# Kernel optimization log

Measured on AMD Instinct MI355X. Metric: run time of the kernel, lower is better.

## Reference

```python
import jax, jax.numpy as jnp
import numpy as np

HID = 1024
HEADS = 16
DH = HID // HEADS
SCALE = DH ** -0.5
L, B = 2048, 2


def setup_inputs() -> dict:
    key = jax.random.key(0)
    ks = jax.random.split(key, 16)
    inp = {
        "query": jax.random.normal(ks[0], (L, B, HID), jnp.float32),
        "key": jax.random.normal(ks[1], (L, B, HID), jnp.float32),
        "value": jax.random.normal(ks[2], (L, B, HID), jnp.float32),
        "mask": jax.random.randint(ks[3], (B, L), 0, 2).astype(bool),
    }
    # xavier-uniform linear weights (torch Linear stores [out, in]; y = x @ W.T + b)
    lim = (6.0 / (HID + HID)) ** 0.5
    for i, name in enumerate(["wq", "wk", "wv", "wfc"]):
        inp[name] = jax.random.uniform(ks[4 + i], (HID, HID), jnp.float32, -lim, lim)
    inp["bq"] = jnp.zeros((HID,), jnp.float32)
    inp["bk"] = jnp.zeros((HID,), jnp.float32)
    inp["bv"] = jnp.zeros((HID,), jnp.float32)
    inp["bfc"] = jnp.zeros((HID,), jnp.float32)
    inp["tao"] = jnp.full((HEADS,), 10.0, jnp.float32)
    return inp


def reference(query, key, value, mask, wq, bq, wk, bk, wv, bv, wfc, bfc, tao):
    # inputs arrive [L, B, D]; module transposes to [B, L, D]
    q = jnp.swapaxes(query, 0, 1)
    k = jnp.swapaxes(key, 0, 1)
    v = jnp.swapaxes(value, 0, 1)
    bsz, length, _ = q.shape

    def heads(x, w, b):
        y = x @ w.T + b                      # [B, L, D]
        return y.reshape(bsz, length, HEADS, DH).transpose(0, 2, 1, 3)  # [B, H, L, d]

    Q = heads(q, wq, bq)
    K = heads(k, wk, bk)
    V = heads(v, wv, bv)

    qk = jnp.einsum("bhqd,bhkd->bhqk", Q, K) * SCALE  # [B, H, L, L]

    # gaussian positional bias: -|i-j|^2/2 * tao_h^-4
    idx = jnp.arange(length, dtype=jnp.float32)
    dist = -0.5 * (idx[:, None] - idx[None, :]) ** 2          # [L, L]
    qk = qk + dist[None, None, :, :] * (tao ** -4)[None, :, None, None]

    qk = jnp.where(mask[:, None, None, :], -jnp.inf, qk)
    attn = jax.nn.softmax(qk, axis=-1)  # dropout is identity in eval mode

    x = jnp.einsum("bhqk,bhkd->bhqd", attn, V)            # [B, H, L, d]
    x = x.transpose(0, 2, 1, 3).reshape(bsz, length, HID)  # [B, L, D]
    x = x @ wfc.T + bfc
    return jnp.swapaxes(x, 0, 1)  # [L, B, D]
```

## Files before the change

### kernel.cpp

```cpp
#include <hip/hip_runtime.h>

#define LQ   2048
#define BQ   2
#define HID  1024
#define NH   16
#define DH   64
#define SCALE 0.125f
#define L2E  1.44269504088896f
#define C1   0.18033688011f
#define EXPOFF 23.0831206542f

using short8  = __attribute__((ext_vector_type(8))) short;
using ushort8 = __attribute__((ext_vector_type(8))) unsigned short;
using f32x4   = __attribute__((ext_vector_type(4))) float;
typedef unsigned short u16;
typedef __attribute__((ext_vector_type(2))) __bf16 bf16x2;

__device__ inline u16 f2bf(float x) {
    unsigned int u = __float_as_uint(x);
    u = (u + 0x7fffu + ((u >> 16) & 1u)) >> 16;
    return (u16)u;
}

#if defined(__has_builtin)
#if __has_builtin(__builtin_amdgcn_cvt_pk_bf16_f32)
#define HAVE_PKBF 1
#endif
#if __has_builtin(__builtin_amdgcn_exp2f)
#define HAVE_EXP2 1
#endif
#endif

__device__ inline unsigned int pkbf(float a, float b) {
#ifdef HAVE_PKBF
    bf16x2 r = __builtin_amdgcn_cvt_pk_bf16_f32(a, b);
    return __builtin_bit_cast(unsigned int, r);
#else
    return (unsigned int)f2bf(a) | ((unsigned int)f2bf(b) << 16);
#endif
}

__device__ inline float fexp2(float x) {
#ifdef HAVE_EXP2
    return __builtin_amdgcn_exp2f(x);
#else
    return exp2f(x);
#endif
}

__device__ inline void gl_lds16(const void* g, void* l) {
    __builtin_amdgcn_global_load_lds(
        (const __attribute__((address_space(1))) void*)g,
        (__attribute__((address_space(3))) void*)l, 16, 0, 0);
}

struct CastArgs {
    const float* s[4];
    u16* d[4];
    int n;
    const unsigned char* mraw;
    int* mout;
    int mn;
};

__global__ __launch_bounds__(256) void castw(CastArgs a) {
    const int y = blockIdx.y;
    const int t = threadIdx.x;
    if (y == 4) {
        if (blockIdx.x != 0) return;
        __shared__ int cnt;
        if (t == 0) cnt = 0;
        __syncthreads();
        int local = 0;
        for (int i = t; i < a.mn; i += 256)
            if ((i & 3) && a.mraw[i]) local++;
        atomicAdd(&cnt, local);
        __syncthreads();
        bool isInt32 = (cnt == 0);
        const int* mi = (const int*)a.mraw;
        for (int i = t; i < a.mn; i += 256)
            a.mout[i] = isInt32 ? mi[i] : (int)a.mraw[i];
        return;
    }
    const float* s = a.s[y];
    u16* d = a.d[y];
    const int n4 = a.n >> 2;
    for (int i = blockIdx.x * 256 + t; i < n4; i += gridDim.x * 256) {
        float4 v = *(const float4*)(s + (size_t)i * 4);
        uint2 p;
        p.x = pkbf(v.x, v.y);
        p.y = pkbf(v.z, v.w);
        *(uint2*)(d + (size_t)i * 4) = p;
    }
}

struct QkvArgs {
    const float* A[3];
    const u16* W[3];
    const float* bias[3];
    u16* out[3];
};

__global__ __launch_bounds__(256) void gemm_qkv(QkvArgs ga) {
    __shared__ float Asf[128][32];
    __shared__ u16 Bs[128][32];

    const int z = blockIdx.z;
    const float* A = ga.A[z];
    const u16* W = ga.W[z];
    const float* bias = ga.bias[z];
    u16* outp = ga.out[z];

    const int t = threadIdx.x;
    const int m0 = blockIdx.x * 128;
    const int n0 = blockIdx.y * 128;
    const int lane = t & 63;
    const int lane15 = lane & 15;
    const int quad = lane >> 4;
    const int w = t >> 6;
    const int wm = (w >> 1) * 64;
    const int wn = (w & 1) * 64;

    const int arow = 8 * w + (lane >> 3);
    const int ach = (lane & 7) ^ ((lane >> 3) & 7);
    const float* aS = A + (size_t)(m0 + arow) * HID + 4 * ach;
    const int brow = 32 * w + (lane >> 2);
    const int bch = (lane & 3) ^ ((lane >> 3) & 3);
    const u16* bS0 = W + (size_t)(n0 + brow) * HID + 8 * bch;
    const u16* bS1 = bS0 + (size_t)16 * HID;
    u16* bD0 = &Bs[32 * w][0];
    u16* bD1 = &Bs[32 * w + 16][0];

    const int sa = lane15 & 7;
    const int qp = quad ^ ((lane15 >> 1) & 3);

    f32x4 acc[4][4];
#pragma unroll
    for (int i = 0; i < 4; i++)
#pragma unroll
        for (int j = 0; j < 4; j++) acc[i][j] = (f32x4){0,0,0,0};

    for (int k0 = 0; k0 < HID; k0 += 32) {
        __syncthreads();
#pragma unroll
        for (int i = 0; i < 4; i++)
            gl_lds16(aS + (size_t)(32 * i) * HID + k0, &Asf[32 * i + (8 * w)][0]);
        gl_lds16(bS0 + k0, bD0);
        gl_lds16(bS1 + k0, bD1);
        __syncthreads();

        short8 af[4], bf[4];
#pragma unroll
        for (int i = 0; i < 4; i++) {
            const float* ap = &Asf[wm + i * 16 + lane15][0];
            const float4 fa = *(const float4*)(ap + 4 * ((2 * quad) ^ sa));
            const float4 fb = *(const float4*)(ap + 4 * ((2 * quad + 1) ^ sa));
            uint4 ui;
            ui.x = pkbf(fa.x, fa.y); ui.y = pkbf(fa.z, fa.w);
            ui.z = pkbf(fb.x, fb.y); ui.w = pkbf(fb.z, fb.w);
            af[i] = __builtin_bit_cast(short8, ui);
            bf[i] = *(const short8*)&Bs[wn + i * 16 + lane15][qp * 8];
        }
#pragma unroll
        for (int mi = 0; mi < 4; mi++)
#pragma unroll
            for (int ni = 0; ni < 4; ni++)
                acc[mi][ni] = __builtin_amdgcn_mfma_f32_16x16x32_bf16(af[mi], bf[ni], acc[mi][ni], 0, 0, 0);
    }

#pragma unroll
    for (int mi = 0; mi < 4; mi++) {
#pragma unroll
        for (int ni = 0; ni < 4; ni++) {
            const int n = n0 + wn + ni * 16 + lane15;
            const float bv = bias[n];
            const int h = n >> 6, d = n & 63;
#pragma unroll
            for (int r = 0; r < 4; r++) {
                const int m = m0 + wm + mi * 16 + quad * 4 + r;
                const float c = acc[mi][ni][r] + bv;
                const int b = m & 1, l = m >> 1;
                if (z < 2) {
                    outp[(((size_t)(b * NH + h)) * LQ + l) * DH + d] = f2bf(c);
                } else {
                    outp[(((size_t)(b * NH + h)) * DH + d) * LQ + l] = f2bf(c);
                }
            }
        }
    }
}

__global__ __launch_bounds__(256) void gemm_fc(const u16* __restrict__ A,
                                               const u16* __restrict__ W,
                                               const float* __restrict__ bias,
                                               float* __restrict__ outp) {
    __shared__ u16 As[128][32];
    __shared__ u16 Bs[64][32];

    const int t = threadIdx.x;
    const int m0 = blockIdx.x * 128;
    const int n0 = blockIdx.y * 64;
    const int lane = t & 63;
    const int lane15 = lane & 15;
    const int quad = lane >> 4;
    const int w = t >> 6;
    const int wm = (w >> 1) * 64;
    const int wn = (w & 1) * 32;

    const int l4 = lane >> 2;
    const int ch = (lane & 3) ^ ((lane >> 3) & 3);
    const u16* aSrc0 = A + (size_t)(m0 + 32 * w + l4) * HID + 8 * ch;
    const u16* aSrc1 = aSrc0 + (size_t)16 * HID;
    const u16* bSrc0 = W + (size_t)(n0 + 16 * w + l4) * HID + 8 * ch;
    u16* aDst0 = &As[32 * w][0];
    u16* aDst1 = &As[32 * w + 16][0];
    u16* bDst0 = &Bs[16 * w][0];

    const int qp = quad ^ ((lane15 >> 1) & 3);

    f32x4 acc[4][2];
#pragma unroll
    for (int i = 0; i < 4; i++)
#pragma unroll
        for (int j = 0; j < 2; j++) acc[i][j] = (f32x4){0,0,0,0};

    for (int k0 = 0; k0 < HID; k0 += 32) {
        __syncthreads();
        gl_lds16(aSrc0 + k0, aDst0);
        gl_lds16(aSrc1 + k0, aDst1);
        gl_lds16(bSrc0 + k0, bDst0);
        __syncthreads();

        short8 af[4], bf[2];
#pragma unroll
        for (int i = 0; i < 4; i++)
            af[i] = *(const short8*)&As[wm + i * 16 + lane15][qp * 8];
#pragma unroll
        for (int j = 0; j < 2; j++)
            bf[j] = *(const short8*)&Bs[wn + j * 16 + lane15][qp * 8];
#pragma unroll
        for (int mi = 0; mi < 4; mi++)
#pragma unroll
            for (int ni = 0; ni < 2; ni++)
                acc[mi][ni] = __builtin_amdgcn_mfma_f32_16x16x32_bf16(af[mi], bf[ni], acc[mi][ni], 0, 0, 0);
    }

#pragma unroll
    for (int mi = 0; mi < 4; mi++) {
#pragma unroll
        for (int ni = 0; ni < 2; ni++) {
            const int n = n0 + wn + ni * 16 + lane15;
            const float bv = bias[n];
#pragma unroll
            for (int r = 0; r < 4; r++) {
                const int m = m0 + wm + mi * 16 + quad * 4 + r;
                outp[(size_t)m * HID + n] = acc[mi][ni][r] + bv;
            }
        }
    }
}

#define PSTR 72

__global__ __launch_bounds__(512) void attn_kernel(const u16* __restrict__ Qg,
                                                   const u16* __restrict__ Kg,
                                                   const u16* __restrict__ Vtg,
                                                   const int* __restrict__ maskI,
                                                   const float* __restrict__ tao,
                                                   u16* __restrict__ Xa) {
    __shared__ u16 Ks[128][64];
    __shared__ u16 Vt[64][128];
    __shared__ u16 PT[128][PSTR];
    __shared__ float smask[128];

    const int bh = blockIdx.x;
    const int q0 = blockIdx.y * 128;
    const int b = bh >> 4;
    const int h = bh & 15;
    const int t = threadIdx.x;
    const int w = t >> 6;
    const int lane = t & 63;
    const int lane15 = lane & 15;
    const int quad = lane >> 4;

    const u16* Kbase = Kg + (size_t)bh * LQ * DH;
    const u16* Vtbase = Vtg + (size_t)bh * DH * LQ;
    const int* mrow = maskI + b * LQ;

    const float tv = tao[h];
    const float t2 = tv * tv;
    const float nb = -0.5f / (t2 * t2);
    const float nb2 = nb * L2E;
    const float skipd2 = -40.0f / nb2;

    const int qrow = q0 + w * 16 + lane15;
    short8 qB0, qB1;
    {
        const u16* qp_ = Qg + ((size_t)bh * LQ + qrow) * DH + quad * 8;
        qB0 = *(const short8*)(qp_);
        qB1 = *(const short8*)(qp_ + 32);
    }

    const int krow = 8 * w + (lane >> 3);
    const int kch = (lane & 7) ^ ((lane >> 3) & 7);
    const u16* kS = Kbase + (size_t)krow * DH + 8 * kch;
    const int vrow = 4 * w + (lane >> 4);
    const int vch = (lane & 8) | ((lane & 7) ^ (vrow & 7));
    const u16* vS = Vtbase + (size_t)vrow * LQ + 8 * vch;
    u16* kD0 = &Ks[8 * w][0];
    u16* kD1 = &Ks[64 + 8 * w][0];
    u16* vD0 = &Vt[4 * w][0];
    u16* vD1 = &Vt[32 + 4 * w][0];

    const int s0 = (quad ^ (lane15 & 7)) * 8;
    const int s1 = ((4 + quad) ^ (lane15 & 7)) * 8;

    f32x4 O[4];
#pragma unroll
    for (int mt = 0; mt < 4; mt++) O[mt] = (f32x4){0,0,0,0};
    float l_ = 0.0f;

    const float ebase0 = (float)(qrow - quad * 4);
    const int prow = w * 16 + lane15;

    for (int k0 = 0; k0 < LQ; k0 += 128) {
        {
            int dmin = 0;
            if (k0 > q0 + 127) dmin = k0 - (q0 + 127);
            else if (k0 + 127 < q0) dmin = q0 - (k0 + 127);
            const float df = (float)dmin;
            if (df * df > skipd2) continue;
        }
        __syncthreads();
        gl_lds16(kS + (size_t)k0 * DH, kD0);
        gl_lds16(kS + (size_t)(k0 + 64) * DH, kD1);
        gl_lds16(vS + k0, vD0);
        gl_lds16(vS + (size_t)32 * LQ + k0, vD1);
        if (t < 128) smask[t] = mrow[k0 + t] ? -3.0e38f : -EXPOFF;
        __syncthreads();

#pragma unroll
        for (int hh = 0; hh < 2; hh++) {
            const int kbase = 64 * hh;
            f32x4 S[4];
#pragma unroll
            for (int kt = 0; kt < 4; kt++) {
                const u16* kr = &Ks[kbase + kt * 16 + lane15][0];
                const short8 ka = *(const short8*)(kr + s0);
                const short8 kb = *(const short8*)(kr + s1);
                S[kt] = __builtin_amdgcn_mfma_f32_16x16x32_bf16(ka, qB0, (f32x4){0,0,0,0}, 0, 0, 0);
                S[kt] = __builtin_amdgcn_mfma_f32_16x16x32_bf16(kb, qB1, S[kt], 0, 0, 0);
            }

            const float ebase = ebase0 - (float)(k0 + kbase);
            float lacc = 0.0f;
#pragma unroll
            for (int kt = 0; kt < 4; kt++) {
                const float4 sm4 = *(const float4*)&smask[kbase + kt * 16 + quad * 4];
                float p[4];
#pragma unroll
                for (int r = 0; r < 4; r++) {
                    const float d = ebase - (float)(kt * 16 + r);
                    const float tb = fmaf(nb2 * d, d, ((const float*)&sm4)[r]);
                    p[r] = fexp2(fmaf(S[kt][r], C1, tb));
                    lacc += p[r];
                }
                uint2 pk2;
                pk2.x = pkbf(p[0], p[1]);
                pk2.y = pkbf(p[2], p[3]);
                *(uint2*)&PT[prow][kt * 16 + quad * 4] = pk2;
            }
            l_ += lacc;

            const short8 pB0 = *(const short8*)&PT[prow][quad * 8];
            const short8 pB1 = *(const short8*)&PT[prow][32 + quad * 8];
#pragma unroll
            for (int mt = 0; mt < 4; mt++) {
                const u16* vr = &Vt[mt * 16 + lane15][kbase];
                const short8 va = *(const short8*)(vr + s0);
                const short8 vb = *(const short8*)(vr + s1);
                O[mt] = __builtin_amdgcn_mfma_f32_16x16x32_bf16(va, pB0, O[mt], 0, 0, 0);
                O[mt] = __builtin_amdgcn_mfma_f32_16x16x32_bf16(vb, pB1, O[mt], 0, 0, 0);
            }
        }
    }

    l_ += __shfl_xor(l_, 16, 64);
    l_ += __shfl_xor(l_, 32, 64);

    {
        const float inv = 1.0f / l_;
        u16* dst = Xa + ((size_t)qrow * BQ + b) * HID + h * DH;
#pragma unroll
        for (int mt = 0; mt < 4; mt++) {
            uint2 pk2;
            pk2.x = pkbf(O[mt][0] * inv, O[mt][1] * inv);
            pk2.y = pkbf(O[mt][2] * inv, O[mt][3] * inv);
            *(uint2*)(dst + mt * 16 + quad * 4) = pk2;
        }
    }
}

extern "C" void kernel_launch(void* const* d_in, const int* in_sizes, int n_in,
                              void* d_out, int out_size, void* d_ws, size_t ws_size,
                              hipStream_t stream) {
    const float* q    = (const float*)d_in[0];
    const float* k    = (const float*)d_in[1];
    const float* v    = (const float*)d_in[2];
    const void*  mask = d_in[3];
    const float* wq   = (const float*)d_in[4];
    const float* wk   = (const float*)d_in[5];
    const float* wv   = (const float*)d_in[6];
    const float* wfc  = (const float*)d_in[7];
    const float* bq   = (const float*)d_in[8];
    const float* bk   = (const float*)d_in[9];
    const float* bv   = (const float*)d_in[10];
    const float* bfc  = (const float*)d_in[11];
    const float* tao  = (const float*)d_in[12];

    const size_t NE = (size_t)LQ * BQ * HID;
    const size_t NW = (size_t)HID * HID;
    u16* base = (u16*)d_ws;
    u16* Qp    = base;
    u16* Kp    = base + NE;
    u16* Vtp   = base + 2 * NE;
    u16* Xa    = base + 3 * NE;
    u16* wqbf  = base + 4 * NE;
    u16* wkbf  = wqbf + NW;
    u16* wvbf  = wkbf + NW;
    u16* wfcbf = wvbf + NW;
    int* maskI = (int*)(wfcbf + NW);

    CastArgs ca;
    ca.s[0] = wq;  ca.d[0] = wqbf;
    ca.s[1] = wk;  ca.d[1] = wkbf;
    ca.s[2] = wv;  ca.d[2] = wvbf;
    ca.s[3] = wfc; ca.d[3] = wfcbf;
    ca.n = (int)NW;
    ca.mraw = (const unsigned char*)mask;
    ca.mout = maskI;
    ca.mn = BQ * LQ;
    castw<<<dim3(256, 5), 256, 0, stream>>>(ca);

    QkvArgs ga;
    ga.A[0] = q;  ga.W[0] = wqbf;  ga.bias[0] = bq;  ga.out[0] = Qp;
    ga.A[1] = k;  ga.W[1] = wkbf;  ga.bias[1] = bk;  ga.out[1] = Kp;
    ga.A[2] = v;  ga.W[2] = wvbf;  ga.bias[2] = bv;  ga.out[2] = Vtp;
    gemm_qkv<<<dim3(32, 8, 3), 256, 0, stream>>>(ga);

    attn_kernel<<<dim3(32, 16), 512, 0, stream>>>(Qp, Kp, Vtp, maskI, tao, Xa);

    gemm_fc<<<dim3(32, 16), 256, 0, stream>>>(Xa, wfcbf, bfc, (float*)d_out);
}
```

Baseline: 245.7 us.

## Pre-cast QKV activations to bf16 and deepen GEMM K-tiles to 64

The q/k/v activations are now converted to bf16 in the existing cast kernel, so the QKV GEMM loads bf16 instead of fp32 and no longer packs to bf16 inside its inner loop. Both the QKV and FC GEMMs move from a K-step of 32 to 64 with a new XOR swizzle, which halves the barrier count and issues two MFMAs per fragment pair. The trade-off is an extra full read and write pass over the activations in the cast kernel, plus more LDS per block.

```diff
diff --git a/kernel.cpp b/kernel.cpp
--- a/kernel.cpp
+++ b/kernel.cpp
@@ -55,9 +55,9 @@
 }
 
 struct CastArgs {
-    const float* s[4];
-    u16* d[4];
-    int n;
+    const float* s[7];
+    u16* d[7];
+    int n[7];
     const unsigned char* mraw;
     int* mout;
     int mn;
@@ -66,7 +66,7 @@
 __global__ __launch_bounds__(256) void castw(CastArgs a) {
     const int y = blockIdx.y;
     const int t = threadIdx.x;
-    if (y == 4) {
+    if (y == 7) {
         if (blockIdx.x != 0) return;
         __shared__ int cnt;
         if (t == 0) cnt = 0;
@@ -84,7 +84,7 @@
     }
     const float* s = a.s[y];
     u16* d = a.d[y];
-    const int n4 = a.n >> 2;
+    const int n4 = a.n[y] >> 2;
     for (int i = blockIdx.x * 256 + t; i < n4; i += gridDim.x * 256) {
         float4 v = *(const float4*)(s + (size_t)i * 4);
         uint2 p;
@@ -95,18 +95,18 @@
 }
 
 struct QkvArgs {
-    const float* A[3];
+    const u16* A[3];
     const u16* W[3];
     const float* bias[3];
     u16* out[3];
 };
 
 __global__ __launch_bounds__(256) void gemm_qkv(QkvArgs ga) {
-    __shared__ float Asf[128][32];
-    __shared__ u16 Bs[128][32];
+    __shared__ u16 As[128][64];
+    __shared__ u16 Bs[128][64];
 
     const int z = blockIdx.z;
-    const float* A = ga.A[z];
+    const u16* A = ga.A[z];
     const u16* W = ga.W[z];
     const float* bias = ga.bias[z];
     u16* outp = ga.out[z];
@@ -121,18 +121,13 @@
     const int wm = (w >> 1) * 64;
     const int wn = (w & 1) * 64;
 
-    const int arow = 8 * w + (lane >> 3);
-    const int ach = (lane & 7) ^ ((lane >> 3) & 7);
-    const float* aS = A + (size_t)(m0 + arow) * HID + 4 * ach;
-    const int brow = 32 * w + (lane >> 2);
-    const int bch = (lane & 3) ^ ((lane >> 3) & 3);
-    const u16* bS0 = W + (size_t)(n0 + brow) * HID + 8 * bch;
-    const u16* bS1 = bS0 + (size_t)16 * HID;
-    u16* bD0 = &Bs[32 * w][0];
-    u16* bD1 = &Bs[32 * w + 16][0];
-
-    const int sa = lane15 & 7;
-    const int qp = quad ^ ((lane15 >> 1) & 3);
+    const int lrow = lane >> 3;
+    const int ch = (lane & 7) ^ ((lane >> 3) & 7);
+    const u16* aS = A + (size_t)(m0 + 32 * w + lrow) * HID + 8 * ch;
+    const u16* bS = W + (size_t)(n0 + 32 * w + lrow) * HID + 8 * ch;
+
+    const int s0 = (quad ^ (lane15 & 7)) * 8;
+    const int s1 = ((4 + quad) ^ (lane15 & 7)) * 8;
 
     f32x4 acc[4][4];
 #pragma unroll
@@ -140,32 +135,32 @@
 #pragma unroll
         for (int j = 0; j < 4; j++) acc[i][j] = (f32x4){0,0,0,0};
 
-    for (int k0 = 0; k0 < HID; k0 += 32) {
-        __syncthreads();
-#pragma unroll
-        for (int i = 0; i < 4; i++)
-            gl_lds16(aS + (size_t)(32 * i) * HID + k0, &Asf[32 * i + (8 * w)][0]);
-        gl_lds16(bS0 + k0, bD0);
-        gl_lds16(bS1 + k0, bD1);
-        __syncthreads();
-
-        short8 af[4], bf[4];
+    for (int k0 = 0; k0 < HID; k0 += 64) {
+        __syncthreads();
 #pragma unroll
         for (int i = 0; i < 4; i++) {
-            const float* ap = &Asf[wm + i * 16 + lane15][0];
-            const float4 fa = *(const float4*)(ap + 4 * ((2 * quad) ^ sa));
-            const float4 fb = *(const float4*)(ap + 4 * ((2 * quad + 1) ^ sa));
-            uint4 ui;
-            ui.x = pkbf(fa.x, fa.y); ui.y = pkbf(fa.z, fa.w);
-            ui.z = pkbf(fb.x, fb.y); ui.w = pkbf(fb.z, fb.w);
-            af[i] = __builtin_bit_cast(short8, ui);
-            bf[i] = *(const short8*)&Bs[wn + i * 16 + lane15][qp * 8];
+            gl_lds16(aS + (size_t)(8 * i) * HID + k0, &As[32 * w + 8 * i][0]);
+            gl_lds16(bS + (size_t)(8 * i) * HID + k0, &Bs[32 * w + 8 * i][0]);
+        }
+        __syncthreads();
+
+        short8 af0[4], af1[4], bf0[4], bf1[4];
+#pragma unroll
+        for (int i = 0; i < 4; i++) {
+            const u16* ar = &As[wm + i * 16 + lane15][0];
+            const u16* br = &Bs[wn + i * 16 + lane15][0];
+            af0[i] = *(const short8*)(ar + s0);
+            af1[i] = *(const short8*)(ar + s1);
+            bf0[i] = *(const short8*)(br + s0);
+            bf1[i] = *(const short8*)(br + s1);
         }
 #pragma unroll
         for (int mi = 0; mi < 4; mi++)
 #pragma unroll
-            for (int ni = 0; ni < 4; ni++)
-                acc[mi][ni] = __builtin_amdgcn_mfma_f32_16x16x32_bf16(af[mi], bf[ni], acc[mi][ni], 0, 0, 0);
+            for (int ni = 0; ni < 4; ni++) {
+                acc[mi][ni] = __builtin_amdgcn_mfma_f32_16x16x32_bf16(af0[mi], bf0[ni], acc[mi][ni], 0, 0, 0);
+                acc[mi][ni] = __builtin_amdgcn_mfma_f32_16x16x32_bf16(af1[mi], bf1[ni], acc[mi][ni], 0, 0, 0);
+            }
     }
 
 #pragma unroll
@@ -194,8 +189,8 @@
                                                const u16* __restrict__ W,
                                                const float* __restrict__ bias,
                                                float* __restrict__ outp) {
-    __shared__ u16 As[128][32];
-    __shared__ u16 Bs[64][32];
+    __shared__ u16 As[128][64];
+    __shared__ u16 Bs[64][64];
 
     const int t = threadIdx.x;
     const int m0 = blockIdx.x * 128;
@@ -207,16 +202,13 @@
     const int wm = (w >> 1) * 64;
     const int wn = (w & 1) * 32;
 
-    const int l4 = lane >> 2;
-    const int ch = (lane & 3) ^ ((lane >> 3) & 3);
-    const u16* aSrc0 = A + (size_t)(m0 + 32 * w + l4) * HID + 8 * ch;
-    const u16* aSrc1 = aSrc0 + (size_t)16 * HID;
-    const u16* bSrc0 = W + (size_t)(n0 + 16 * w + l4) * HID + 8 * ch;
-    u16* aDst0 = &As[32 * w][0];
-    u16* aDst1 = &As[32 * w + 16][0];
-    u16* bDst0 = &Bs[16 * w][0];
-
-    const int qp = quad ^ ((lane15 >> 1) & 3);
+    const int lrow = lane >> 3;
+    const int ch = (lane & 7) ^ ((lane >> 3) & 7);
+    const u16* aS = A + (size_t)(m0 + 32 * w + lrow) * HID + 8 * ch;
+    const u16* bS = W + (size_t)(n0 + 16 * w + lrow) * HID + 8 * ch;
+
+    const int s0 = (quad ^ (lane15 & 7)) * 8;
+    const int s1 = ((4 + quad) ^ (lane15 & 7)) * 8;
 
     f32x4 acc[4][2];
 #pragma unroll
@@ -224,25 +216,36 @@
 #pragma unroll
         for (int j = 0; j < 2; j++) acc[i][j] = (f32x4){0,0,0,0};
 
-    for (int k0 = 0; k0 < HID; k0 += 32) {
-        __syncthreads();
-        gl_lds16(aSrc0 + k0, aDst0);
-        gl_lds16(aSrc1 + k0, aDst1);
-        gl_lds16(bSrc0 + k0, bDst0);
-        __syncthreads();
-
-        short8 af[4], bf[2];
+    for (int k0 = 0; k0 < HID; k0 += 64) {
+        __syncthreads();
 #pragma unroll
         for (int i = 0; i < 4; i++)
-            af[i] = *(const short8*)&As[wm + i * 16 + lane15][qp * 8];
-#pragma unroll
-        for (int j = 0; j < 2; j++)
-            bf[j] = *(const short8*)&Bs[wn + j * 16 + lane15][qp * 8];
+            gl_lds16(aS + (size_t)(8 * i) * HID + k0, &As[32 * w + 8 * i][0]);
+#pragma unroll
+        for (int i = 0; i < 2; i++)
+            gl_lds16(bS + (size_t)(8 * i) * HID + k0, &Bs[16 * w + 8 * i][0]);
+        __syncthreads();
+
+        short8 af0[4], af1[4], bf0[2], bf1[2];
+#pragma unroll
+        for (int i = 0; i < 4; i++) {
+            const u16* ar = &As[wm + i * 16 + lane15][0];
+            af0[i] = *(const short8*)(ar + s0);
+            af1[i] = *(const short8*)(ar + s1);
+        }
+#pragma unroll
+        for (int j = 0; j < 2; j++) {
+            const u16* br = &Bs[wn + j * 16 + lane15][0];
+            bf0[j] = *(const short8*)(br + s0);
+            bf1[j] = *(const short8*)(br + s1);
+        }
 #pragma unroll
         for (int mi = 0; mi < 4; mi++)
 #pragma unroll
-            for (int ni = 0; ni < 2; ni++)
-                acc[mi][ni] = __builtin_amdgcn_mfma_f32_16x16x32_bf16(af[mi], bf[ni], acc[mi][ni], 0, 0, 0);
+            for (int ni = 0; ni < 2; ni++) {
+                acc[mi][ni] = __builtin_amdgcn_mfma_f32_16x16x32_bf16(af0[mi], bf0[ni], acc[mi][ni], 0, 0, 0);
+                acc[mi][ni] = __builtin_amdgcn_mfma_f32_16x16x32_bf16(af1[mi], bf1[ni], acc[mi][ni], 0, 0, 0);
+            }
     }
 
 #pragma unroll
@@ -425,27 +428,32 @@
     u16* Kp    = base + NE;
     u16* Vtp   = base + 2 * NE;
     u16* Xa    = base + 3 * NE;
-    u16* wqbf  = base + 4 * NE;
+    u16* qbf   = base + 4 * NE;
+    u16* kbf   = base + 5 * NE;
+    u16* vbf   = base + 6 * NE;
+    u16* wqbf  = base + 7 * NE;
     u16* wkbf  = wqbf + NW;
     u16* wvbf  = wkbf + NW;
     u16* wfcbf = wvbf + NW;
     int* maskI = (int*)(wfcbf + NW);
 
     CastArgs ca;
-    ca.s[0] = wq;  ca.d[0] = wqbf;
-    ca.s[1] = wk;  ca.d[1] = wkbf;
-    ca.s[2] = wv;  ca.d[2] = wvbf;
-    ca.s[3] = wfc; ca.d[3] = wfcbf;
-    ca.n = (int)NW;
+    ca.s[0] = q;   ca.d[0] = qbf;   ca.n[0] = (int)NE;
+    ca.s[1] = k;   ca.d[1] = kbf;   ca.n[1] = (int)NE;
+    ca.s[2] = v;   ca.d[2] = vbf;   ca.n[2] = (int)NE;
+    ca.s[3] = wq;  ca.d[3] = wqbf;  ca.n[3] = (int)NW;
+    ca.s[4] = wk;  ca.d[4] = wkbf;  ca.n[4] = (int)NW;
+    ca.s[5] = wv;  ca.d[5] = wvbf;  ca.n[5] = (int)NW;
+    ca.s[6] = wfc; ca.d[6] = wfcbf; ca.n[6] = (int)NW;
     ca.mraw = (const unsigned char*)mask;
     ca.mout = maskI;
     ca.mn = BQ * LQ;
-    castw<<<dim3(256, 5), 256, 0, stream>>>(ca);
+    castw<<<dim3(256, 8), 256, 0, stream>>>(ca);
 
     QkvArgs ga;
-    ga.A[0] = q;  ga.W[0] = wqbf;  ga.bias[0] = bq;  ga.out[0] = Qp;
-    ga.A[1] = k;  ga.W[1] = wkbf;  ga.bias[1] = bk;  ga.out[1] = Kp;
-    ga.A[2] = v;  ga.W[2] = wvbf;  ga.bias[2] = bv;  ga.out[2] = Vtp;
+    ga.A[0] = qbf;  ga.W[0] = wqbf;  ga.bias[0] = bq;  ga.out[0] = Qp;
+    ga.A[1] = kbf;  ga.W[1] = wkbf;  ga.bias[1] = bk;  ga.out[1] = Kp;
+    ga.A[2] = vbf;  ga.W[2] = wvbf;  ga.bias[2] = bv;  ga.out[2] = Vtp;
     gemm_qkv<<<dim3(32, 8, 3), 256, 0, stream>>>(ga);
 
     attn_kernel<<<dim3(32, 16), 512, 0, stream>>>(Qp, Kp, Vtp, maskI, tao, Xa);
```

After: 233.1 us. -5.1%, faster.
